# Kernel optimization log

Hardware: AMD Instinct MI355X
Metric: run time of the kernel (lower is better)

The kernel has to match this reference:

```python
import jax, jax.numpy as jnp
import numpy as np

TEMPERATURE = 0.07
EPS = 1e-8  # torch CosineSimilarity norm clamp

N, D, NUM_CLASSES = 4096, 768, 128


def setup_inputs() -> dict:
    key = jax.random.key(0)
    k1, k2, k3 = jax.random.split(key, 3)
    img_emb = jax.random.normal(k1, (N, D), dtype=jnp.float32)
    text_emb = jax.random.normal(k2, (N, D), dtype=jnp.float32)
    labels = jax.random.randint(k3, (N,), 0, NUM_CLASSES, dtype=jnp.int64)
    return {"img_emb": img_emb, "text_emb": text_emb, "labels": labels}


def reference(img_emb, text_emb, labels):
    # cosine similarity via normalize + matmul (avoids O(N^2 D) broadcast)
    img_n = img_emb / jnp.maximum(jnp.linalg.norm(img_emb, axis=-1, keepdims=True), EPS)
    txt_n = text_emb / jnp.maximum(jnp.linalg.norm(text_emb, axis=-1, keepdims=True), EPS)
    logits = jnp.einsum('id,jd->ij', img_n, txt_n) / TEMPERATURE  # [N, N]

    pos_mask = (labels[:, None] == labels[None, :]).astype(logits.dtype)  # [N, N]

    img2text = -(pos_mask * jax.nn.log_softmax(logits, axis=1)).sum(1).mean()
    text2img = -(pos_mask * jax.nn.log_softmax(logits, axis=0)).sum(0).mean()
    return (img2text + text2img) / 2
```

## Files before the change

### kernel.cpp

```cpp
#include <hip/hip_runtime.h>
#include <hip/hip_bf16.h>

#define N_ 4096
#define D_ 768
#define NCLS 128
#define BM 128
#define BN 128
#define BK 64
#define NSTEP 12

typedef __bf16 bf16x8 __attribute__((ext_vector_type(8)));
typedef float f32x4 __attribute__((ext_vector_type(4)));
typedef short s16x8 __attribute__((ext_vector_type(8)));

__global__ __launch_bounds__(192) void normalize_kernel(
    const float* __restrict__ img, const float* __restrict__ txt,
    __hip_bfloat16* __restrict__ img_nb, __hip_bfloat16* __restrict__ txt_nb,
    double* __restrict__ accs, unsigned* __restrict__ cnt) {
  int b = blockIdx.x;
  if (b == 0 && threadIdx.x == 0) {
    accs[0] = 0.0;
    accs[1] = 0.0;
    *cnt = 0u;
  }
  const float* s;
  __hip_bfloat16* d;
  if (b < N_) {
    s = img + (size_t)b * D_;
    d = img_nb + (size_t)b * D_;
  } else {
    s = txt + (size_t)(b - N_) * D_;
    d = txt_nb + (size_t)(b - N_) * D_;
  }
  int tid = threadIdx.x;
  float4 v = ((const float4*)s)[tid];
  float ss = v.x * v.x + v.y * v.y + v.z * v.z + v.w * v.w;
#pragma unroll
  for (int m = 32; m; m >>= 1) ss += __shfl_xor(ss, m);
  __shared__ float wsum[3];
  int lane = tid & 63, w = tid >> 6;
  if (lane == 0) wsum[w] = ss;
  __syncthreads();
  float inv = 1.0f / fmaxf(sqrtf(wsum[0] + wsum[1] + wsum[2]), 1e-8f);
  ushort4 o;
  o.x = __bfloat16_as_ushort(__float2bfloat16(v.x * inv));
  o.y = __bfloat16_as_ushort(__float2bfloat16(v.y * inv));
  o.z = __bfloat16_as_ushort(__float2bfloat16(v.z * inv));
  o.w = __bfloat16_as_ushort(__float2bfloat16(v.w * inv));
  ((ushort4*)d)[tid] = o;
}

__global__ __launch_bounds__(256) void gemm_epi_kernel(
    const unsigned short* __restrict__ A, const unsigned short* __restrict__ B,
    const int* __restrict__ labels, float* __restrict__ row_part,
    float* __restrict__ col_part, float* __restrict__ S_part) {
  __shared__ __align__(16) unsigned short As[2][8192];
  __shared__ __align__(16) unsigned short Bs[2][8192];
  __shared__ int labR[BM], labC[BN];
  __shared__ float rbuf[2][BM], cbuf[2][BN];
  __shared__ float sbuf[4];

  const int lin = blockIdx.y * 32 + blockIdx.x;
  const int xcd = lin & 7, idx = lin >> 3;
  const int bx = xcd * 4 + (idx & 3), by = idx >> 2;

  const int tid = threadIdx.x;
  const int lane = tid & 63, wave = tid >> 6;
  const int wr = wave >> 1, wc = wave & 1;
  const int g = lane >> 4, fr = lane & 15;
  const int rowBase = by * BM, colBase = bx * BN;

  if (tid < BM) labR[tid] = labels[rowBase + tid];
  else labC[tid - BM] = labels[colBase + tid - BM];

  const int gq = tid & 7, rbase = tid >> 3;
  const unsigned short* pa = A + (size_t)(rowBase + rbase) * D_ + gq * 8;
  const unsigned short* pb = B + (size_t)(colBase + rbase) * D_ + gq * 8;
  const int wpos = (rbase * 8 + (gq ^ (rbase & 7))) * 8;

  f32x4 acc[4][4] = {};

  s16x8 ra[4], rb[4];
#pragma unroll
  for (int j = 0; j < 4; ++j) {
    ra[j] = *(const s16x8*)(pa + (size_t)(32 * j) * D_);
    rb[j] = *(const s16x8*)(pb + (size_t)(32 * j) * D_);
  }
#pragma unroll
  for (int j = 0; j < 4; ++j) {
    *(s16x8*)&As[0][wpos + j * 2048] = ra[j];
    *(s16x8*)&Bs[0][wpos + j * 2048] = rb[j];
  }
#pragma unroll
  for (int j = 0; j < 4; ++j) {
    ra[j] = *(const s16x8*)(pa + (size_t)(32 * j) * D_ + BK);
    rb[j] = *(const s16x8*)(pb + (size_t)(32 * j) * D_ + BK);
  }
  __syncthreads();

  for (int u = 0; u < NSTEP; ++u) {
    const unsigned short* as_ = As[u & 1];
    const unsigned short* bs_ = Bs[u & 1];
    bf16x8 af[4], bf[4];
    {
      const int sw = g ^ (fr & 7);
#pragma unroll
      for (int m = 0; m < 4; ++m)
        af[m] = *(const bf16x8*)&as_[((wr * 64 + m * 16 + fr) * 8 + sw) * 8];
#pragma unroll
      for (int n = 0; n < 4; ++n)
        bf[n] = *(const bf16x8*)&bs_[((wc * 64 + n * 16 + fr) * 8 + sw) * 8];
    }
    if (u + 1 < NSTEP) {
      unsigned short* aw = As[(u + 1) & 1];
      unsigned short* bw = Bs[(u + 1) & 1];
#pragma unroll
      for (int j = 0; j < 4; ++j) {
        *(s16x8*)&aw[wpos + j * 2048] = ra[j];
        *(s16x8*)&bw[wpos + j * 2048] = rb[j];
      }
    }
#pragma unroll
    for (int m = 0; m < 4; ++m)
#pragma unroll
      for (int n = 0; n < 4; ++n)
        acc[m][n] = __builtin_amdgcn_mfma_f32_16x16x32_bf16(af[m], bf[n], acc[m][n], 0, 0, 0);
    {
      const int sw = (4 + g) ^ (fr & 7);
#pragma unroll
      for (int m = 0; m < 4; ++m)
        af[m] = *(const bf16x8*)&as_[((wr * 64 + m * 16 + fr) * 8 + sw) * 8];
#pragma unroll
      for (int n = 0; n < 4; ++n)
        bf[n] = *(const bf16x8*)&bs_[((wc * 64 + n * 16 + fr) * 8 + sw) * 8];
    }
#pragma unroll
    for (int m = 0; m < 4; ++m)
#pragma unroll
      for (int n = 0; n < 4; ++n)
        acc[m][n] = __builtin_amdgcn_mfma_f32_16x16x32_bf16(af[m], bf[n], acc[m][n], 0, 0, 0);
    if (u + 2 < NSTEP) {
      const int k0 = (u + 2) * BK;
#pragma unroll
      for (int j = 0; j < 4; ++j) {
        ra[j] = *(const s16x8*)(pa + (size_t)(32 * j) * D_ + k0);
        rb[j] = *(const s16x8*)(pb + (size_t)(32 * j) * D_ + k0);
      }
    }
    __syncthreads();
  }

  const float scale = 14.285714285714286f;
  float sPart = 0.f;
  float colAcc[4] = {0.f, 0.f, 0.f, 0.f};
#pragma unroll
  for (int m = 0; m < 4; ++m) {
    float ra2[4] = {0.f, 0.f, 0.f, 0.f};
#pragma unroll
    for (int n = 0; n < 4; ++n) {
      int col = wc * 64 + n * 16 + fr;
      int lc = labC[col];
#pragma unroll
      for (int r = 0; r < 4; ++r) {
        float v = acc[m][n][r] * scale;
        float e = __expf(v);
        ra2[r] += e;
        colAcc[n] += e;
        int row = wr * 64 + m * 16 + g * 4 + r;
        if (labR[row] == lc) sPart += v;
      }
    }
#pragma unroll
    for (int r = 0; r < 4; ++r) {
      float x = ra2[r];
      x += __shfl_xor(x, 1);
      x += __shfl_xor(x, 2);
      x += __shfl_xor(x, 4);
      x += __shfl_xor(x, 8);
      if (fr == 0) rbuf[wc][wr * 64 + m * 16 + g * 4 + r] = x;
    }
  }
#pragma unroll
  for (int n = 0; n < 4; ++n) {
    float x = colAcc[n];
    x += __shfl_xor(x, 16);
    x += __shfl_xor(x, 32);
    if (g == 0) cbuf[wr][wc * 64 + n * 16 + fr] = x;
  }
  float s = sPart;
#pragma unroll
  for (int m = 32; m; m >>= 1) s += __shfl_xor(s, m);
  if (lane == 0) sbuf[wave] = s;
  __syncthreads();
  if (tid < BM)
    row_part[(size_t)bx * N_ + rowBase + tid] = rbuf[0][tid] + rbuf[1][tid];
  else
    col_part[(size_t)by * N_ + colBase + (tid - BM)] = cbuf[0][tid - BM] + cbuf[1][tid - BM];
  if (tid == 0) S_part[by * 32 + bx] = sbuf[0] + sbuf[1] + sbuf[2] + sbuf[3];
}

__global__ __launch_bounds__(256) void reduce_kernel(
    const float* __restrict__ row_part, const float* __restrict__ col_part,
    const float* __restrict__ S_part, const int* __restrict__ labels,
    double* __restrict__ accs, unsigned* __restrict__ cnt, float* __restrict__ out) {
  __shared__ int hist[NCLS];
  int tid = threadIdx.x;
  if (tid < NCLS) hist[tid] = 0;
  __syncthreads();
  for (int j = tid; j < N_; j += 256) atomicAdd(&hist[labels[j]], 1);
  __syncthreads();

  int i = blockIdx.x * 256 + tid;
  float rs = 0.f, cs = 0.f;
#pragma unroll
  for (int b = 0; b < 32; ++b) {
    rs += row_part[(size_t)b * N_ + i];
    cs += col_part[(size_t)b * N_ + i];
  }
  int c = hist[labels[i]];
  double term = (double)c * ((double)logf(rs) + (double)logf(cs));
  double sterm = (i < 1024) ? (double)S_part[i] : 0.0;
#pragma unroll
  for (int m = 32; m; m >>= 1) {
    term += __shfl_xor(term, m);
    sterm += __shfl_xor(sterm, m);
  }
  __shared__ double tbuf[4], sb[4];
  int lane = tid & 63, w = tid >> 6;
  if (lane == 0) { tbuf[w] = term; sb[w] = sterm; }
  __syncthreads();
  if (tid == 0) {
    atomicAdd(&accs[0], tbuf[0] + tbuf[1] + tbuf[2] + tbuf[3]);
    atomicAdd(&accs[1], sb[0] + sb[1] + sb[2] + sb[3]);
    __threadfence();
    unsigned old = atomicAdd(cnt, 1u);
    if (old == 15u) {
      double t = atomicAdd(&accs[0], 0.0);
      double s2 = atomicAdd(&accs[1], 0.0);
      out[0] = (float)((t - 2.0 * s2) / (2.0 * (double)N_));
    }
  }
}

extern "C" void kernel_launch(void* const* d_in, const int* in_sizes, int n_in,
                              void* d_out, int out_size, void* d_ws, size_t ws_size,
                              hipStream_t stream) {
  const float* img = (const float*)d_in[0];
  const float* txt = (const float*)d_in[1];
  const int* labels = (const int*)d_in[2];
  float* out = (float*)d_out;
  char* ws = (char*)d_ws;

  __hip_bfloat16* img_nb = (__hip_bfloat16*)(ws);
  __hip_bfloat16* txt_nb = (__hip_bfloat16*)(ws + 6291456);
  float* row_part = (float*)(ws + 12582912);
  float* col_part = (float*)(ws + 13107200);
  float* S_part = (float*)(ws + 13631488);
  double* accs = (double*)(ws + 13635584);
  unsigned* cnt = (unsigned*)(ws + 13635600);

  normalize_kernel<<<2 * N_, 192, 0, stream>>>(img, txt, img_nb, txt_nb, accs, cnt);
  gemm_epi_kernel<<<dim3(32, 32), 256, 0, stream>>>(
      (const unsigned short*)img_nb, (const unsigned short*)txt_nb, labels,
      row_part, col_part, S_part);
  reduce_kernel<<<16, 256, 0, stream>>>(row_part, col_part, S_part, labels, accs, cnt, out);
}
```

Before: 53.94 us.

## Stream GEMM tiles directly into LDS with global_load_lds double buffering

Replaces register-staged global loads plus LDS stores with direct global-to-LDS 16-byte loads, moving the XOR swizzle onto the source address. A two-stage pipeline uses explicit s_barrier and vmcnt waits, so the next tile's loads are in flight while the current one is computed. This cuts VGPR pressure and the ds_write instructions. In exchange the loads are only one stage ahead instead of two, and the last iteration issues a redundant reload into the other buffer.

```diff
diff --git a/kernel.cpp b/kernel.cpp
--- a/kernel.cpp
+++ b/kernel.cpp
@@ -11,7 +11,16 @@
 
 typedef __bf16 bf16x8 __attribute__((ext_vector_type(8)));
 typedef float f32x4 __attribute__((ext_vector_type(4)));
-typedef short s16x8 __attribute__((ext_vector_type(8)));
+
+#define SBAR() asm volatile("s_barrier" ::: "memory")
+#define VMWAIT8() asm volatile("s_waitcnt vmcnt(8)" ::: "memory")
+#define LGKM0() asm volatile("s_waitcnt lgkmcnt(0)" ::: "memory")
+
+__device__ __forceinline__ void gload16(const unsigned short* g, unsigned short* l) {
+  __builtin_amdgcn_global_load_lds(
+      (const __attribute__((address_space(1))) unsigned int*)g,
+      (__attribute__((address_space(3))) unsigned int*)l, 16, 0, 0);
+}
 
 __global__ __launch_bounds__(192) void normalize_kernel(
     const float* __restrict__ img, const float* __restrict__ txt,
@@ -72,83 +81,57 @@
 
   if (tid < BM) labR[tid] = labels[rowBase + tid];
   else labC[tid - BM] = labels[colBase + tid - BM];
-
-  const int gq = tid & 7, rbase = tid >> 3;
-  const unsigned short* pa = A + (size_t)(rowBase + rbase) * D_ + gq * 8;
-  const unsigned short* pb = B + (size_t)(colBase + rbase) * D_ + gq * 8;
-  const int wpos = (rbase * 8 + (gq ^ (rbase & 7))) * 8;
+  __syncthreads();
+
+  const int r0 = lane >> 3;
+  const int cswz = (lane & 7) ^ (r0 & 7);
+  const unsigned short* pa = A + (size_t)(rowBase + wave * 8 + r0) * D_ + cswz * 8;
+  const unsigned short* pb = B + (size_t)(colBase + wave * 8 + r0) * D_ + cswz * 8;
+  const int dbase = wave * 8 * 64;
+
+#pragma unroll
+  for (int j = 0; j < 4; ++j) {
+    gload16(pa + (size_t)(32 * j) * D_, &As[0][dbase + j * 2048]);
+    gload16(pb + (size_t)(32 * j) * D_, &Bs[0][dbase + j * 2048]);
+  }
 
   f32x4 acc[4][4] = {};
 
-  s16x8 ra[4], rb[4];
-#pragma unroll
-  for (int j = 0; j < 4; ++j) {
-    ra[j] = *(const s16x8*)(pa + (size_t)(32 * j) * D_);
-    rb[j] = *(const s16x8*)(pb + (size_t)(32 * j) * D_);
-  }
-#pragma unroll
-  for (int j = 0; j < 4; ++j) {
-    *(s16x8*)&As[0][wpos + j * 2048] = ra[j];
-    *(s16x8*)&Bs[0][wpos + j * 2048] = rb[j];
-  }
-#pragma unroll
-  for (int j = 0; j < 4; ++j) {
-    ra[j] = *(const s16x8*)(pa + (size_t)(32 * j) * D_ + BK);
-    rb[j] = *(const s16x8*)(pb + (size_t)(32 * j) * D_ + BK);
-  }
-  __syncthreads();
-
   for (int u = 0; u < NSTEP; ++u) {
+    SBAR();
+    {
+      const int su = (u + 1 < NSTEP) ? u + 1 : u;
+      const size_t kk = (size_t)su * BK;
+      const int sl = (u + 1) & 1;
+#pragma unroll
+      for (int j = 0; j < 4; ++j) {
+        gload16(pa + (size_t)(32 * j) * D_ + kk, &As[sl][dbase + j * 2048]);
+        gload16(pb + (size_t)(32 * j) * D_ + kk, &Bs[sl][dbase + j * 2048]);
+      }
+    }
+    VMWAIT8();
+    SBAR();
     const unsigned short* as_ = As[u & 1];
     const unsigned short* bs_ = Bs[u & 1];
-    bf16x8 af[4], bf[4];
-    {
-      const int sw = g ^ (fr & 7);
+#pragma unroll
+    for (int ks = 0; ks < 2; ++ks) {
+      const int sw = (ks * 4 + g) ^ (fr & 7);
+      bf16x8 af[4], bf[4];
 #pragma unroll
       for (int m = 0; m < 4; ++m)
         af[m] = *(const bf16x8*)&as_[((wr * 64 + m * 16 + fr) * 8 + sw) * 8];
 #pragma unroll
       for (int n = 0; n < 4; ++n)
         bf[n] = *(const bf16x8*)&bs_[((wc * 64 + n * 16 + fr) * 8 + sw) * 8];
-    }
-    if (u + 1 < NSTEP) {
-      unsigned short* aw = As[(u + 1) & 1];
-      unsigned short* bw = Bs[(u + 1) & 1];
-#pragma unroll
-      for (int j = 0; j < 4; ++j) {
-        *(s16x8*)&aw[wpos + j * 2048] = ra[j];
-        *(s16x8*)&bw[wpos + j * 2048] = rb[j];
-      }
-    }
-#pragma unroll
-    for (int m = 0; m < 4; ++m)
-#pragma unroll
-      for (int n = 0; n < 4; ++n)
-        acc[m][n] = __builtin_amdgcn_mfma_f32_16x16x32_bf16(af[m], bf[n], acc[m][n], 0, 0, 0);
-    {
-      const int sw = (4 + g) ^ (fr & 7);
 #pragma unroll
       for (int m = 0; m < 4; ++m)
-        af[m] = *(const bf16x8*)&as_[((wr * 64 + m * 16 + fr) * 8 + sw) * 8];
-#pragma unroll
-      for (int n = 0; n < 4; ++n)
-        bf[n] = *(const bf16x8*)&bs_[((wc * 64 + n * 16 + fr) * 8 + sw) * 8];
-    }
-#pragma unroll
-    for (int m = 0; m < 4; ++m)
-#pragma unroll
-      for (int n = 0; n < 4; ++n)
-        acc[m][n] = __builtin_amdgcn_mfma_f32_16x16x32_bf16(af[m], bf[n], acc[m][n], 0, 0, 0);
-    if (u + 2 < NSTEP) {
-      const int k0 = (u + 2) * BK;
-#pragma unroll
-      for (int j = 0; j < 4; ++j) {
-        ra[j] = *(const s16x8*)(pa + (size_t)(32 * j) * D_ + k0);
-        rb[j] = *(const s16x8*)(pb + (size_t)(32 * j) * D_ + k0);
-      }
-    }
-    __syncthreads();
-  }
+#pragma unroll
+        for (int n = 0; n < 4; ++n)
+          acc[m][n] = __builtin_amdgcn_mfma_f32_16x16x32_bf16(af[m], bf[n], acc[m][n], 0, 0, 0);
+    }
+    LGKM0();
+  }
+  __syncthreads();
 
   const float scale = 14.285714285714286f;
   float sPart = 0.f;
```

New measurement: 53.91 us. About the same (-0.1%).
